# Optimization experiments

Hardware: AMD Instinct MI355X
Metric: run time of the kernel (lower is better)

## Reference

```python
import jax, jax.numpy as jnp
from jax import lax
import numpy as np

# --- module constants (from __init__ defaults) ---
SRADIUS = 9                      # spatial_radius
RRADIUS = 0.5                    # range_radius
MAX_ITER = 3                     # max_iteration
SDIAM = 2 * SRADIUS + 1          # 19
PI = 3.141592653589793
SSIGMA = float(np.sqrt(2 * SRADIUS ** 2) / 1.5)
RNG_THR = float(np.exp(-0.5) / (RRADIUS * np.sqrt(2 * PI)))  # gaussian value at |diff|==rradius


def _gaussian(x, sigma):
    return jnp.exp(-0.5 * (x / sigma) ** 2) / (sigma * np.sqrt(2 * PI))


def _spatial_weights():
    # spt_kernel[y, x] = dist to center, flattened row-major -> channel index y*SDIAM + x
    ax, ay = np.meshgrid(np.arange(SDIAM), np.arange(SDIAM))
    d = np.sqrt((ax - SRADIUS) ** 2 + (ay - SRADIUS) ** 2).reshape(-1)
    w = np.exp(-0.5 * (d / SSIGMA) ** 2) / (SSIGMA * np.sqrt(2 * PI))
    return jnp.asarray(w, jnp.float32)[None, :, None, None]  # [1, 361, 1, 1]


def _neighbor_patches(x):
    # Equivalent to conv2d(ReplicationPad2d(x), one-hot nei_kernel): channel c = value of
    # neighbor at offset (c // SDIAM - r, c % SDIAM - r). Patch channel ordering matches
    # the torch kernel's row-major (y*SDIAM + x) indexing since C==1.
    xp = jnp.pad(x, ((0, 0), (0, 0), (SRADIUS, SRADIUS), (SRADIUS, SRADIUS)), mode='edge')
    return lax.conv_general_dilated_patches(xp, (SDIAM, SDIAM), (1, 1), 'VALID')  # [bs, 361, ht, wd]


def setup_inputs() -> dict:
    key = jax.random.key(0)
    features = jax.random.uniform(key, (2, 1, 192, 192), dtype=jnp.float32)
    return {"features": features}


def reference(features):
    spt_wght = _spatial_weights()
    x = features  # [bs, 1, ht, wd]
    for _ in range(MAX_ITER):
        nei_x = _neighbor_patches(x)                 # [bs, 361, ht, wd] neighbor values
        diff = x - nei_x                             # rng_kernel = center - neighbor (0 at center tap)
        rng_w = jnp.maximum(_gaussian(diff, RRADIUS) - RNG_THR, 0.0)  # linear-map so w(|diff|>rradius)=0
        w = rng_w * spt_wght                         # spatial * range weights
        x = (w * nei_x).sum(axis=1, keepdims=True) / (w.sum(axis=1, keepdims=True) + 1e-8)
    return x
```

## Files before the change

### kernel.cpp

```cpp
#include <hip/hip_runtime.h>

#define SR   9
#define SD   19
#define TW   16
#define TH   6
#define LW   (TW + 2*SR)
#define LH   (TH + 2*SR)
#define LS   42
#define IMG  192
#define NPIX (IMG*IMG)

__global__ __launch_bounds__(384) void ms_iter(const float* __restrict__ in,
                                               float* __restrict__ out) {
    __shared__ __align__(16) float tile[LH * LS];
    __shared__ float4 part[8][48];

    const int b   = blockIdx.z;
    const int bx0 = blockIdx.x * TW;
    const int by0 = blockIdx.y * TH;
    const float* __restrict__ img = in + b * NPIX;

    const int tid = threadIdx.x;
    const int tz  = tid / 48;
    const int s   = tid - 48 * tz;
    const int tx  = s & 7;
    const int ty  = s >> 3;

    for (int i = tid; i < LH * LW; i += 384) {
        int r  = i / LW, c = i - r * LW;
        int gy = min(max(by0 + r - SR, 0), IMG - 1);
        int gx = min(max(bx0 + c - SR, 0), IMG - 1);
        tile[r * LS + c] = img[gy * IMG + gx];
    }
    __syncthreads();

    constexpr float CX[SD] = {
        0.5697829f, 0.6411806f, 0.7115726f, 0.7788008f, 0.8406238f,
        0.8948393f, 0.9394131f, 0.9726045f, 0.9930797f, 1.0000000f,
        0.9930797f, 0.9726045f, 0.9394131f, 0.8948393f, 0.8406238f,
        0.7788008f, 0.7115726f, 0.6411806f, 0.5697829f
    };
    const float a3 = -0.8285240f, a2 = 1.5534825f, a1 = -1.5923197f, a0 = 0.3138366f;

    const int   x0 = 2 * tx;
    const float cA = tile[(ty + SR) * LS + x0 + SR];
    const float cB = tile[(ty + SR) * LS + x0 + SR + 1];

    const int beg = (tz < 3) ? 3 * tz : (9 + 2 * (tz - 3));
    const int nr  = (tz < 3) ? 3 : 2;

    float numA = 0.f, denA = 0.f, numB = 0.f, denB = 0.f;
    for (int r = 0; r < nr; ++r) {
        const int   dy = beg + r;
        const float ft = (float)(dy - SR);
        const float fy = __builtin_amdgcn_exp2f(ft * ft * -0.010018715f);

        const float2* r2 = reinterpret_cast<const float2*>(&tile[(ty + dy) * LS + x0]);
        float w[20];
#pragma unroll
        for (int j = 0; j < 10; ++j) { float2 v = r2[j]; w[2*j] = v.x; w[2*j+1] = v.y; }

        float rnA = 0.f, rdA = 0.f, rnB = 0.f, rdB = 0.f;
#pragma unroll
        for (int dx = 0; dx < SD; ++dx) {
            float nA = w[dx], nB = w[dx + 1];
            float dA = cA - nA,      dB = cB - nB;
            float tA = dA * dA,      tB = dB * dB;
            float uA = fmaf(tA, a3, a2);
            float uB = fmaf(tB, a3, a2);
            uA = fmaf(uA, tA, a1);   uB = fmaf(uB, tB, a1);
            uA = fmaf(uA, tA, a0);   uB = fmaf(uB, tB, a0);
            float wA = fminf(fmaxf(uA * CX[dx], 0.f), 1.f);
            float wB = fminf(fmaxf(uB * CX[dx], 0.f), 1.f);
            rnA = fmaf(wA, nA, rnA);
            rnB = fmaf(wB, nB, rnB);
            rdA += wA;               rdB += wB;
        }
        numA = fmaf(fy, rnA, numA); denA = fmaf(fy, rdA, denA);
        numB = fmaf(fy, rnB, numB); denB = fmaf(fy, rdB, denB);
    }

    part[tz][s] = make_float4(numA, denA, numB, denB);
    __syncthreads();

    if (tid < 48) {
        float nA = 0.f, dA = 0.f, nB = 0.f, dB = 0.f;
#pragma unroll
        for (int g = 0; g < 8; ++g) {
            float4 v = part[g][tid];
            nA += v.x; dA += v.y; nB += v.z; dB += v.w;
        }
        const float K = 0.04701581f;
        float2 o;
        o.x = (K * nA) / (K * dA + 1e-8f);
        o.y = (K * nB) / (K * dB + 1e-8f);
        const int otx = tid & 7, oty = tid >> 3;
        *reinterpret_cast<float2*>(&out[b * NPIX + (by0 + oty) * IMG + bx0 + 2 * otx]) = o;
    }
}

extern "C" void kernel_launch(void* const* d_in, const int* in_sizes, int n_in,
                              void* d_out, int out_size, void* d_ws, size_t ws_size,
                              hipStream_t stream) {
    const float* in  = (const float*)d_in[0];
    float*       out = (float*)d_out;
    float*       ws  = (float*)d_ws;

    dim3 grid(IMG / TW, IMG / TH, 2);
    dim3 block(384, 1, 1);

    ms_iter<<<grid, block, 0, stream>>>(in, out);
    ms_iter<<<grid, block, 0, stream>>>(out, ws);
    ms_iter<<<grid, block, 0, stream>>>(ws, out);
}
```

Measured before the change: 26.44 us.

## Switch inner bilateral loop to packed fp16 math with 4 pixels per thread

Stores the shared tile as fp16 and evaluates the range-weight polynomial with packed half2 ops, expanding it around the center value so each tap needs fewer operations. Each thread now handles 4 pixels, and the tile shape changes to 24x4 with 16 row-groups, so partial sums go through separate num/den shared buffers. The intent is to roughly halve ALU work per tap through packed fp16 math. In exchange, weights and per-row accumulation are computed in half precision, which risks accuracy loss against the fp32 reference, especially across 19-term row sums.

After: 29.82 us. 1.13x slower.

```diff
diff --git a/kernel.cpp b/kernel.cpp
--- a/kernel.cpp
+++ b/kernel.cpp
@@ -1,19 +1,22 @@
 #include <hip/hip_runtime.h>
+#include <hip/hip_fp16.h>
 
 #define SR   9
 #define SD   19
-#define TW   16
-#define TH   6
+#define TW   24
+#define TH   4
 #define LW   (TW + 2*SR)
 #define LH   (TH + 2*SR)
-#define LS   42
+#define LSH  48
 #define IMG  192
 #define NPIX (IMG*IMG)
 
+typedef __fp16 h2 __attribute__((ext_vector_type(2)));
+
 __global__ __launch_bounds__(384) void ms_iter(const float* __restrict__ in,
                                                float* __restrict__ out) {
-    __shared__ __align__(16) float tile[LH * LS];
-    __shared__ float4 part[8][48];
+    __shared__ __align__(16) __fp16 tile[LH * LSH];
+    __shared__ float4 pnum[16][24], pden[16][24];
 
     const int b   = blockIdx.z;
     const int bx0 = blockIdx.x * TW;
@@ -21,81 +24,120 @@
     const float* __restrict__ img = in + b * NPIX;
 
     const int tid = threadIdx.x;
-    const int tz  = tid / 48;
-    const int s   = tid - 48 * tz;
-    const int tx  = s & 7;
-    const int ty  = s >> 3;
+    const int tz  = tid / 24;
+    const int s   = tid - 24 * tz;
+    const int qx  = s % 6;
+    const int ty  = s / 6;
 
     for (int i = tid; i < LH * LW; i += 384) {
         int r  = i / LW, c = i - r * LW;
         int gy = min(max(by0 + r - SR, 0), IMG - 1);
         int gx = min(max(bx0 + c - SR, 0), IMG - 1);
-        tile[r * LS + c] = img[gy * IMG + gx];
+        tile[r * LSH + c] = (__fp16)img[gy * IMG + gx];
     }
     __syncthreads();
 
-    constexpr float CX[SD] = {
+    constexpr float CXf[SD] = {
         0.5697829f, 0.6411806f, 0.7115726f, 0.7788008f, 0.8406238f,
         0.8948393f, 0.9394131f, 0.9726045f, 0.9930797f, 1.0000000f,
         0.9930797f, 0.9726045f, 0.9394131f, 0.8948393f, 0.8406238f,
         0.7788008f, 0.7115726f, 0.6411806f, 0.5697829f
     };
-    const float a3 = -0.8285240f, a2 = 1.5534825f, a1 = -1.5923197f, a0 = 0.3138366f;
+    const float a3 = -0.8285240f;
 
-    const int   x0 = 2 * tx;
-    const float cA = tile[(ty + SR) * LS + x0 + SR];
-    const float cB = tile[(ty + SR) * LS + x0 + SR + 1];
+    const int x0 = 4 * qx;
+    float c[4];
+#pragma unroll
+    for (int p = 0; p < 4; ++p)
+        c[p] = (float)tile[(ty + SR) * LSH + x0 + SR + p];
 
-    const int beg = (tz < 3) ? 3 * tz : (9 + 2 * (tz - 3));
-    const int nr  = (tz < 3) ? 3 : 2;
+    float m2c[4], c2[4], c1[4], c0[4];
+#pragma unroll
+    for (int p = 0; p < 4; ++p) {
+        float k = c[p] * c[p];
+        m2c[p] = -2.f * c[p];
+        c2[p]  = k * -2.4855720f + 1.5534825f;
+        c1[p]  = (k * -2.4855720f + 3.1069650f) * k + -1.5923197f;
+        c0[p]  = ((k * a3 + 1.5534825f) * k + -1.5923197f) * k + 0.3138366f;
+    }
+    const h2 m2c01 = __builtin_amdgcn_cvt_pkrtz(m2c[0], m2c[1]);
+    const h2 m2c23 = __builtin_amdgcn_cvt_pkrtz(m2c[2], m2c[3]);
+    const h2 c2_01 = __builtin_amdgcn_cvt_pkrtz(c2[0], c2[1]);
+    const h2 c2_23 = __builtin_amdgcn_cvt_pkrtz(c2[2], c2[3]);
+    const h2 c1_01 = __builtin_amdgcn_cvt_pkrtz(c1[0], c1[1]);
+    const h2 c1_23 = __builtin_amdgcn_cvt_pkrtz(c1[2], c1[3]);
+    const h2 c0_01 = __builtin_amdgcn_cvt_pkrtz(c0[0], c0[1]);
+    const h2 c0_23 = __builtin_amdgcn_cvt_pkrtz(c0[2], c0[3]);
+    const h2 a3_2  = { (__fp16)(-0.8285240f), (__fp16)(-0.8285240f) };
+    const h2 zero2 = { (__fp16)0.f, (__fp16)0.f };
 
-    float numA = 0.f, denA = 0.f, numB = 0.f, denB = 0.f;
-    for (int r = 0; r < nr; ++r) {
-        const int   dy = beg + r;
+    const int beg = (tz < 3) ? 2 * tz : (tz + 3);
+
+    float num[4] = {0.f, 0.f, 0.f, 0.f}, den[4] = {0.f, 0.f, 0.f, 0.f};
+
+    auto row_body = [&](int dy) {
         const float ft = (float)(dy - SR);
         const float fy = __builtin_amdgcn_exp2f(ft * ft * -0.010018715f);
 
-        const float2* r2 = reinterpret_cast<const float2*>(&tile[(ty + dy) * LS + x0]);
-        float w[20];
+        const uint2* q2 = reinterpret_cast<const uint2*>(&tile[(ty + dy) * LSH + x0]);
+        unsigned hp[12];
 #pragma unroll
-        for (int j = 0; j < 10; ++j) { float2 v = r2[j]; w[2*j] = v.x; w[2*j+1] = v.y; }
+        for (int j = 0; j < 6; ++j) { uint2 v = q2[j]; hp[2*j] = v.x; hp[2*j+1] = v.y; }
+        unsigned al[10];
+#pragma unroll
+        for (int j = 0; j < 10; ++j)
+            al[j] = __builtin_amdgcn_alignbit(hp[j + 1], hp[j], 16);
 
-        float rnA = 0.f, rdA = 0.f, rnB = 0.f, rdB = 0.f;
+        h2 rn01 = zero2, rd01 = zero2, rn23 = zero2, rd23 = zero2;
 #pragma unroll
         for (int dx = 0; dx < SD; ++dx) {
-            float nA = w[dx], nB = w[dx + 1];
-            float dA = cA - nA,      dB = cB - nB;
-            float tA = dA * dA,      tB = dB * dB;
-            float uA = fmaf(tA, a3, a2);
-            float uB = fmaf(tB, a3, a2);
-            uA = fmaf(uA, tA, a1);   uB = fmaf(uB, tB, a1);
-            uA = fmaf(uA, tA, a0);   uB = fmaf(uB, tB, a0);
-            float wA = fminf(fmaxf(uA * CX[dx], 0.f), 1.f);
-            float wB = fminf(fmaxf(uB * CX[dx], 0.f), 1.f);
-            rnA = fmaf(wA, nA, rnA);
-            rnB = fmaf(wB, nB, rnB);
-            rdA += wA;               rdB += wB;
+            unsigned u01 = (dx & 1) ? al[dx >> 1] : hp[dx >> 1];
+            unsigned u23 = (dx & 1) ? al[(dx >> 1) + 1] : hp[(dx >> 1) + 1];
+            h2 n01 = __builtin_bit_cast(h2, u01);
+            h2 n23 = __builtin_bit_cast(h2, u23);
+            h2 cx  = { (__fp16)CXf[dx], (__fp16)CXf[dx] };
+
+            h2 t01 = m2c01 * n01 + n01 * n01;
+            h2 t23 = m2c23 * n23 + n23 * n23;
+            h2 p01 = a3_2 * t01 + c2_01;
+            h2 p23 = a3_2 * t23 + c2_23;
+            p01 = p01 * t01 + c1_01;  p23 = p23 * t23 + c1_23;
+            p01 = p01 * t01 + c0_01;  p23 = p23 * t23 + c0_23;
+            h2 w01 = __builtin_elementwise_max(p01 * cx, zero2);
+            h2 w23 = __builtin_elementwise_max(p23 * cx, zero2);
+            rn01 = w01 * n01 + rn01;  rd01 = rd01 + w01;
+            rn23 = w23 * n23 + rn23;  rd23 = rd23 + w23;
         }
-        numA = fmaf(fy, rnA, numA); denA = fmaf(fy, rdA, denA);
-        numB = fmaf(fy, rnB, numB); denB = fmaf(fy, rdB, denB);
-    }
+        num[0] += fy * (float)rn01[0];  den[0] += fy * (float)rd01[0];
+        num[1] += fy * (float)rn01[1];  den[1] += fy * (float)rd01[1];
+        num[2] += fy * (float)rn23[0];  den[2] += fy * (float)rd23[0];
+        num[3] += fy * (float)rn23[1];  den[3] += fy * (float)rd23[1];
+    };
 
-    part[tz][s] = make_float4(numA, denA, numB, denB);
+    row_body(beg);
+    if (tz < 3) row_body(beg + 1);
+
+    pnum[tz][s] = make_float4(num[0], num[1], num[2], num[3]);
+    pden[tz][s] = make_float4(den[0], den[1], den[2], den[3]);
     __syncthreads();
 
-    if (tid < 48) {
-        float nA = 0.f, dA = 0.f, nB = 0.f, dB = 0.f;
+    if (tid < 24) {
+        float4 n = make_float4(0.f, 0.f, 0.f, 0.f);
+        float4 d = make_float4(0.f, 0.f, 0.f, 0.f);
 #pragma unroll
-        for (int g = 0; g < 8; ++g) {
-            float4 v = part[g][tid];
-            nA += v.x; dA += v.y; nB += v.z; dB += v.w;
+        for (int g = 0; g < 16; ++g) {
+            float4 a = pnum[g][tid], e = pden[g][tid];
+            n.x += a.x; n.y += a.y; n.z += a.z; n.w += a.w;
+            d.x += e.x; d.y += e.y; d.z += e.z; d.w += e.w;
         }
         const float K = 0.04701581f;
-        float2 o;
-        o.x = (K * nA) / (K * dA + 1e-8f);
-        o.y = (K * nB) / (K * dB + 1e-8f);
-        const int otx = tid & 7, oty = tid >> 3;
-        *reinterpret_cast<float2*>(&out[b * NPIX + (by0 + oty) * IMG + bx0 + 2 * otx]) = o;
+        float4 o;
+        o.x = (K * n.x) / (K * d.x + 1e-8f);
+        o.y = (K * n.y) / (K * d.y + 1e-8f);
+        o.z = (K * n.z) / (K * d.z + 1e-8f);
+        o.w = (K * n.w) / (K * d.w + 1e-8f);
+        const int oqx = tid % 6, oty = tid / 6;
+        *reinterpret_cast<float4*>(&out[b * NPIX + (by0 + oty) * IMG + bx0 + 4 * oqx]) = o;
     }
 }
 
```
